# Kernel tuning notes

Measured on AMD Instinct MI355X. Metric: run time of the kernel, lower is better.

## Reference

```python
import jax, jax.numpy as jnp
import numpy as np

N = 50000   # graph nodes (== num_edges of road network, Embedding vocab)
E = 800000  # message-passing edges
F = 64      # static_feat_dim
H = 256     # hidden_dim
ID = 32     # id_embed_dim
DYN = 16    # dyn_feat_dim
B = 256
T = 128
STEPS = 3   # gcn_iter


def setup_inputs():
    key = jax.random.key(0)
    it = iter(jax.random.split(key, 48))

    def nrm(shape, fan_in):
        return jax.random.normal(next(it), shape, jnp.float32) / np.sqrt(fan_in)

    edge_src = jax.random.randint(next(it), (E,), 0, N)
    edge_dst = jax.random.randint(next(it), (E,), 0, N)
    lengths = jax.random.randint(next(it), (B,), T // 2, T + 1)
    traj = jax.random.randint(next(it), (B, T), 1, N)
    mask = jnp.arange(T)[None, :] < lengths[:, None]
    traj = jnp.where(mask, traj, 0)  # padding idx 0 past length
    x0 = jax.random.normal(next(it), (N, F), jnp.float32)
    dyn_feat = jax.random.normal(next(it), (B, DYN), jnp.float32)
    Din = H + ID + DYN
    z = lambda *s: jnp.zeros(s, jnp.float32)
    inp = dict(
        x0=x0, dyn_feat=dyn_feat,
        Wproj=nrm((F, H), F), bproj=z(H),
        Wz=nrm((F + H, H), F + H), bz=z(H),
        Wr=nrm((F + H, H), F + H), br=z(H),
        Wn=nrm((F + H, H), F + H), bn=z(H),
        id_emb=nrm((N, ID), 1.0).at[0].set(0.0),  # padding_idx=0
        film_W1=nrm((DYN, H), DYN), film_b1=z(H),
        film_W2=nrm((H, 2 * H), H), film_b2=z(2 * H),
        gru_Wi_f=nrm((Din, 3 * H), Din), gru_Wh_f=nrm((H, 3 * H), H),
        gru_bi_f=z(3 * H), gru_bh_f=z(3 * H),
        gru_Wi_b=nrm((Din, 3 * H), Din), gru_Wh_b=nrm((H, 3 * H), H),
        gru_bi_b=z(3 * H), gru_bh_b=z(3 * H),
        ln_g=jnp.ones((2 * H,), jnp.float32), ln_b=z(2 * H),
        attn_W1=nrm((2 * H + DYN, H), 2 * H + DYN), attn_b1=z(H),
        attn_W2=nrm((H, 1), H), attn_b2=z(1),
        gate_W=nrm((4 * H + DYN, 2 * H), 4 * H + DYN), gate_b=z(2 * H),
        fc_W1=nrm((2 * H + DYN, H), 2 * H + DYN), fc_b1=z(H),
        fc_W2=nrm((H, 1), H), fc_b2=z(1),
        traj=traj, lengths=lengths, edge_src=edge_src, edge_dst=edge_dst)
    return inp


def _run_gru(x, mask, Wi, Wh, bi, bh):
    # x: [B,T,D]; mask: [B,T] bool. Returns (outs [B,T,H] zeroed past length,
    # h_last [B,H] = state at last valid step), matching packed torch GRU.
    xg = jnp.einsum('btd,dh->bth', x, Wi) + bi  # precompute input gates
    Hd = Wh.shape[0]

    def step(h, inp):
        gx, m = inp
        gh = h @ Wh + bh
        xr, xz, xn = jnp.split(gx, 3, axis=-1)
        hr, hz, hn = jnp.split(gh, 3, axis=-1)
        r = jax.nn.sigmoid(xr + hr)
        zt = jax.nn.sigmoid(xz + hz)
        n = jnp.tanh(xn + r * hn)
        h_new = (1 - zt) * n + zt * h
        m2 = m[:, None]
        h = jnp.where(m2, h_new, h)
        return h, h * m2

    h0 = jnp.zeros((x.shape[0], Hd), x.dtype)
    h_last, outs = jax.lax.scan(step, h0, (jnp.swapaxes(xg, 0, 1), mask.T))
    return jnp.swapaxes(outs, 0, 1), h_last


def _forward(x0, dyn_feat, Wproj, bproj, Wz, bz, Wr, br, Wn, bn, id_emb,
             film_W1, film_b1, film_W2, film_b2,
             gru_Wi_f, gru_Wh_f, gru_bi_f, gru_bh_f,
             gru_Wi_b, gru_Wh_b, gru_bi_b, gru_bh_b,
             ln_g, ln_b, attn_W1, attn_b1, attn_W2, attn_b2,
             gate_W, gate_b, fc_W1, fc_b1, fc_W2, fc_b2,
             traj, lengths, edge_src, edge_dst):
    # --- GGNN message passing: scatter-add aggregation + gated update ---
    h = jnp.tanh(x0 @ Wproj + bproj)  # [N,H]
    for _ in range(STEPS):
        h_agg = jax.ops.segment_sum(h[edge_src], edge_dst, num_segments=N)
        xc = jnp.concatenate([x0, h_agg], axis=1)
        zg = jax.nn.sigmoid(xc @ Wz + bz)
        rg = jax.nn.sigmoid(xc @ Wr + br)
        h_t = jnp.tanh(jnp.concatenate([x0, rg * h_agg], axis=1) @ Wn + bn)
        h = (1 - zg) * h_agg + zg * h_t
    # --- FiLM-modulated trajectory sequence ---
    x_seq = h[traj]  # [B,T,H]
    film = jnp.tanh((dyn_feat @ film_W1 + film_b1) @ film_W2 + film_b2)
    g, b = jnp.split(film, 2, axis=-1)
    x_seq = x_seq * (1 + g[:, None, :]) + b[:, None, :]
    dyn_exp = jnp.broadcast_to(dyn_feat[:, None, :], (B, T, DYN))
    rnn_in = jnp.concatenate([x_seq, id_emb[traj], dyn_exp], axis=-1)
    mask = jnp.arange(T)[None, :] < lengths[:, None]
    # --- BiGRU over packed (length-masked) sequences ---
    out_f, h_f = _run_gru(rnn_in, mask, gru_Wi_f, gru_Wh_f, gru_bi_f, gru_bh_f)
    rev = jnp.maximum(lengths[:, None] - 1 - jnp.arange(T)[None, :], 0)  # [B,T]
    x_rev = jnp.take_along_axis(rnn_in, rev[..., None], axis=1)
    out_rb, h_b = _run_gru(x_rev, mask, gru_Wi_b, gru_Wh_b, gru_bi_b, gru_bh_b)
    out_b = jnp.take_along_axis(out_rb, rev[..., None], axis=1) * mask[..., None]
    rnn_out = jnp.concatenate([out_f, out_b], axis=-1)  # [B,T,2H]
    h_last = jnp.concatenate([h_f, h_b], axis=1)        # [B,2H]
    mu = h_last.mean(-1, keepdims=True)
    var = ((h_last - mu) ** 2).mean(-1, keepdims=True)
    rnn_last = (h_last - mu) / jnp.sqrt(var + 1e-5) * ln_g + ln_b
    # --- attention pooling over valid steps ---
    score_in = jnp.concatenate([rnn_out, dyn_exp], axis=-1)
    scores = (jnp.tanh(score_in @ attn_W1 + attn_b1) @ attn_W2 + attn_b2)[..., 0]
    scores = jnp.where(traj != 0, scores, -1e9)
    alpha = jax.nn.softmax(scores, axis=1)[..., None]
    context = (rnn_out * alpha).sum(axis=1)
    # --- fusion gate + head ---
    gate_in = jnp.concatenate([context, rnn_last, dyn_feat], axis=1)
    zf = jax.nn.sigmoid(gate_in @ gate_W + gate_b)
    final = zf * context + (1 - zf) * rnn_last
    hfc = jax.nn.gelu(jnp.concatenate([final, dyn_feat], axis=1) @ fc_W1 + fc_b1,
                      approximate=False)
    return (hfc @ fc_W2 + fc_b2)[:, 0]


def reference(x0, dyn_feat, Wproj, bproj, Wz, bz, Wr, br, Wn, bn, id_emb,
              film_W1, film_b1, film_W2, film_b2,
              gru_Wi_f, gru_Wh_f, gru_bi_f, gru_bh_f,
              gru_Wi_b, gru_Wh_b, gru_bi_b, gru_bh_b,
              ln_g, ln_b, attn_W1, attn_b1, attn_W2, attn_b2,
              gate_W, gate_b, fc_W1, fc_b1, fc_W2, fc_b2,
              traj, lengths, edge_src, edge_dst):
    return _forward(x0, dyn_feat, Wproj, bproj, Wz, bz, Wr, br, Wn, bn, id_emb,
                    film_W1, film_b1, film_W2, film_b2,
                    gru_Wi_f, gru_Wh_f, gru_bi_f, gru_bh_f,
                    gru_Wi_b, gru_Wh_b, gru_bi_b, gru_bh_b,
                    ln_g, ln_b, attn_W1, attn_b1, attn_W2, attn_b2,
                    gate_W, gate_b, fc_W1, fc_b1, fc_W2, fc_b2,
                    traj, lengths, edge_src, edge_dst)
```

## Files before the change

kernel.cpp:

```cpp
#include <hip/hip_runtime.h>
#include <hip/hip_fp16.h>
#include <cmath>

#define NN   50000
#define EE   800000
#define FF   64
#define HH   256
#define IDD  32
#define DYNN 16
#define BB   256
#define TT   128
#define DIN  304
#define G3   768
#define NQ   (HH/4)
#define NQG  ((FF+HH)/4)
#define NQX  (DIN/4)

typedef _Float16 h2_t __attribute__((ext_vector_type(2)));
__device__ __forceinline__ float sigf(float x){ return 1.0f/(1.0f+expf(-x)); }
__device__ __forceinline__ float fdot2(__half2 a, __half2 b, float c) {
    return __builtin_amdgcn_fdot2(*reinterpret_cast<h2_t*>(&a),
                                  *reinterpret_cast<h2_t*>(&b), c, false);
}

#define NPB 16
__global__ __launch_bounds__(256) void k_proj(
    const float* __restrict__ x0, const float* __restrict__ Wproj,
    const float* __restrict__ bproj, float* __restrict__ h,
    __half* __restrict__ h16)
{
    __shared__ float xs[NPB][FF];
    int n0 = blockIdx.x * NPB;
    int j  = threadIdx.x;
    for (int i = j; i < NPB*FF; i += 256) {
        int m = i / FF, k = i % FF;
        int n = n0 + m;
        xs[m][k] = (n < NN) ? x0[n*FF + k] : 0.f;
    }
    __syncthreads();
    float acc[NPB];
#pragma unroll
    for (int m = 0; m < NPB; ++m) acc[m] = 0.f;
    for (int k = 0; k < FF; ++k) {
        float w = Wproj[k*HH + j];
#pragma unroll
        for (int m = 0; m < NPB; ++m) acc[m] += xs[m][k]*w;
    }
    float b = bproj[j];
#pragma unroll
    for (int m = 0; m < NPB; ++m) {
        int n = n0 + m;
        if (n < NN) {
            float v = tanhf(acc[m] + b);
            h[(size_t)n*HH + j] = v;
            h16[(size_t)n*HH + j] = __float2half(v);
        }
    }
}

__global__ __launch_bounds__(768) void k_wt2(
    const float* __restrict__ Wh, __half2* __restrict__ Wq)
{
    int q = blockIdx.x;
    int j = threadIdx.x;
    float w0 = Wh[(size_t)(4*q+0)*G3 + j];
    float w1 = Wh[(size_t)(4*q+1)*G3 + j];
    float w2 = Wh[(size_t)(4*q+2)*G3 + j];
    float w3 = Wh[(size_t)(4*q+3)*G3 + j];
    Wq[((size_t)q*G3 + j)*2 + 0] = __floats2half2_rn(w0, w1);
    Wq[((size_t)q*G3 + j)*2 + 1] = __floats2half2_rn(w2, w3);
}

__global__ __launch_bounds__(256) void k_wtg(
    const float* __restrict__ W, float2* __restrict__ Wq)
{
    int q = blockIdx.x;
    int j = threadIdx.x;
    __half2 a = __floats2half2_rn(W[(size_t)(4*q+0)*HH + j], W[(size_t)(4*q+1)*HH + j]);
    __half2 b = __floats2half2_rn(W[(size_t)(4*q+2)*HH + j], W[(size_t)(4*q+3)*HH + j]);
    float2 o;
    reinterpret_cast<__half2*>(&o)[0] = a;
    reinterpret_cast<__half2*>(&o)[1] = b;
    Wq[(size_t)q*HH + j] = o;
}

__global__ __launch_bounds__(768) void k_wti(
    const float* __restrict__ Wi, float2* __restrict__ Wq)
{
    int q = blockIdx.x;
    int j = threadIdx.x;
    __half2 a = __floats2half2_rn(Wi[(size_t)(4*q+0)*G3 + j], Wi[(size_t)(4*q+1)*G3 + j]);
    __half2 b = __floats2half2_rn(Wi[(size_t)(4*q+2)*G3 + j], Wi[(size_t)(4*q+3)*G3 + j]);
    float2 o;
    reinterpret_cast<__half2*>(&o)[0] = a;
    reinterpret_cast<__half2*>(&o)[1] = b;
    Wq[(size_t)q*G3 + j] = o;
}

__global__ __launch_bounds__(256) void k_hist(
    const int* __restrict__ dst, int* __restrict__ cnt)
{
    int e = blockIdx.x*256 + threadIdx.x;
    if (e < EE) atomicAdd(&cnt[dst[e]], 1);
}

__global__ __launch_bounds__(1024) void k_prefix(
    const int* __restrict__ cnt, int* __restrict__ offs)
{
    __shared__ int sm[1024];
    __shared__ int carry;
    int j = threadIdx.x;
    if (j == 0) carry = 0;
    __syncthreads();
    for (int base = 0; base < NN; base += 1024) {
        int v = (base + j < NN) ? cnt[base + j] : 0;
        sm[j] = v; __syncthreads();
        for (int s = 1; s < 1024; s <<= 1) {
            int t = (j >= s) ? sm[j - s] : 0;
            __syncthreads();
            sm[j] += t;
            __syncthreads();
        }
        int inc = sm[j];
        int c = carry;
        if (base + j < NN) offs[base + j] = c + inc - v;
        __syncthreads();
        if (j == 1023) carry = c + sm[1023];
        __syncthreads();
    }
    if (j == 0) offs[NN] = carry;
}

__global__ __launch_bounds__(256) void k_fill(
    const int* __restrict__ src, const int* __restrict__ dst,
    const int* __restrict__ offs, int* __restrict__ cur,
    int* __restrict__ srcb)
{
    int e = blockIdx.x*256 + threadIdx.x;
    if (e < EE) {
        int d = dst[e];
        int p = atomicAdd(&cur[d], 1);
        srcb[offs[d] + p] = src[e];
    }
}

#define APB 4
__global__ __launch_bounds__(256) void k_aggregate(
    const __half* __restrict__ h16, const int* __restrict__ offs,
    const int* __restrict__ srcb, float* __restrict__ hagg)
{
    int w    = threadIdx.x >> 6;
    int lane = threadIdx.x & 63;
    int half = lane >> 5;
    int l32  = lane & 31;
    int n = blockIdx.x * APB + w;
    if (n >= NN) return;
    int e0 = offs[n], e1 = offs[n+1];
    float acc[8];
#pragma unroll
    for (int k = 0; k < 8; ++k) acc[k] = 0.f;
    int e = e0;
    for (; e + 8 <= e1; e += 8) {
        int sA = srcb[e     + half];
        int sB = srcb[e + 2 + half];
        int sC = srcb[e + 4 + half];
        int sD = srcb[e + 6 + half];
        float4 rA = *reinterpret_cast<const float4*>(&h16[(size_t)sA*HH + l32*8]);
        float4 rB = *reinterpret_cast<const float4*>(&h16[(size_t)sB*HH + l32*8]);
        float4 rC = *reinterpret_cast<const float4*>(&h16[(size_t)sC*HH + l32*8]);
        float4 rD = *reinterpret_cast<const float4*>(&h16[(size_t)sD*HH + l32*8]);
        const __half2* hA = reinterpret_cast<const __half2*>(&rA);
        const __half2* hB = reinterpret_cast<const __half2*>(&rB);
        const __half2* hC = reinterpret_cast<const __half2*>(&rC);
        const __half2* hD = reinterpret_cast<const __half2*>(&rD);
#pragma unroll
        for (int k = 0; k < 4; ++k) {
            float2 a = __half22float2(hA[k]);
            float2 b = __half22float2(hB[k]);
            float2 c = __half22float2(hC[k]);
            float2 d = __half22float2(hD[k]);
            acc[2*k]   += (a.x + b.x) + (c.x + d.x);
            acc[2*k+1] += (a.y + b.y) + (c.y + d.y);
        }
    }
    for (; e + 2 <= e1; e += 2) {
        int s = srcb[e + half];
        float4 r = *reinterpret_cast<const float4*>(&h16[(size_t)s*HH + l32*8]);
        const __half2* hp = reinterpret_cast<const __half2*>(&r);
#pragma unroll
        for (int k = 0; k < 4; ++k) {
            float2 a = __half22float2(hp[k]);
            acc[2*k] += a.x; acc[2*k+1] += a.y;
        }
    }
    if (e < e1 && half == 0) {
        int s = srcb[e];
        float4 r = *reinterpret_cast<const float4*>(&h16[(size_t)s*HH + l32*8]);
        const __half2* hp = reinterpret_cast<const __half2*>(&r);
#pragma unroll
        for (int k = 0; k < 4; ++k) {
            float2 a = __half22float2(hp[k]);
            acc[2*k] += a.x; acc[2*k+1] += a.y;
        }
    }
#pragma unroll
    for (int k = 0; k < 8; ++k) acc[k] += __shfl_xor(acc[k], 32, 64);
    if (half == 0) {
        float4 o0 = {acc[0], acc[1], acc[2], acc[3]};
        float4 o1 = {acc[4], acc[5], acc[6], acc[7]};
        float4* dst = reinterpret_cast<float4*>(&hagg[(size_t)n*HH + l32*8]);
        dst[0] = o0; dst[1] = o1;
    }
}

__global__ __launch_bounds__(256) void k_gnn_update(
    const float* __restrict__ x0, const float* __restrict__ hagg,
    const float2* __restrict__ wqz, const float2* __restrict__ wqr,
    const float2* __restrict__ wqn,
    const float* __restrict__ bz, const float* __restrict__ br,
    const float* __restrict__ bn, float* __restrict__ h,
    __half* __restrict__ h16)
{
    __shared__ __align__(16) __half inh[NPB][FF+HH];
    __shared__ __align__(16) __half rhh[NPB][HH];
    __shared__ float hsf[NPB][HH];
    int n0 = blockIdx.x * NPB;
    int j  = threadIdx.x;
    for (int i = j; i < NPB*FF; i += 256) {
        int m = i >> 6, k = i & 63;
        int n = n0 + m;
        inh[m][k] = __float2half((n < NN) ? x0[n*FF + k] : 0.f);
    }
#pragma unroll
    for (int m = 0; m < NPB; ++m) {
        int n = n0 + m;
        float hv = (n < NN) ? hagg[(size_t)n*HH + j] : 0.f;
        hsf[m][j] = hv;
        inh[m][FF + j] = __float2half(hv);
    }
    __syncthreads();

    float az[NPB], ar[NPB];
#pragma unroll
    for (int m = 0; m < NPB; ++m) { az[m] = 0.f; ar[m] = 0.f; }
    for (int q = 0; q < NQG; ++q) {
        float2 wzr = wqz[(size_t)q*HH + j];
        float2 wrr = wqr[(size_t)q*HH + j];
        __half2 wz01 = reinterpret_cast<__half2*>(&wzr)[0];
        __half2 wz23 = reinterpret_cast<__half2*>(&wzr)[1];
        __half2 wr01 = reinterpret_cast<__half2*>(&wrr)[0];
        __half2 wr23 = reinterpret_cast<__half2*>(&wrr)[1];
#pragma unroll
        for (int m = 0; m < NPB; ++m) {
            float2 hraw = *reinterpret_cast<const float2*>(&inh[m][4*q]);
            __half2 h01 = reinterpret_cast<__half2*>(&hraw)[0];
            __half2 h23 = reinterpret_cast<__half2*>(&hraw)[1];
            az[m] = fdot2(h01, wz01, az[m]); az[m] = fdot2(h23, wz23, az[m]);
            ar[m] = fdot2(h01, wr01, ar[m]); ar[m] = fdot2(h23, wr23, ar[m]);
        }
    }
    float bzj = bz[j], brj = br[j];
    float zg[NPB];
#pragma unroll
    for (int m = 0; m < NPB; ++m) {
        zg[m] = sigf(az[m] + bzj);
        float rg = sigf(ar[m] + brj);
        rhh[m][j] = __float2half(rg * hsf[m][j]);
    }
    __syncthreads();
    float an[NPB];
#pragma unroll
    for (int m = 0; m < NPB; ++m) an[m] = 0.f;
    for (int q = 0; q < FF/4; ++q) {
        float2 wnr = wqn[(size_t)q*HH + j];
        __half2 wn01 = reinterpret_cast<__half2*>(&wnr)[0];
        __half2 wn23 = reinterpret_cast<__half2*>(&wnr)[1];
#pragma unroll
        for (int m = 0; m < NPB; ++m) {
            float2 hraw = *reinterpret_cast<const float2*>(&inh[m][4*q]);
            __half2 h01 = reinterpret_cast<__half2*>(&hraw)[0];
            __half2 h23 = reinterpret_cast<__half2*>(&hraw)[1];
            an[m] = fdot2(h01, wn01, an[m]); an[m] = fdot2(h23, wn23, an[m]);
        }
    }
    for (int q = FF/4; q < NQG; ++q) {
        float2 wnr = wqn[(size_t)q*HH + j];
        __half2 wn01 = reinterpret_cast<__half2*>(&wnr)[0];
        __half2 wn23 = reinterpret_cast<__half2*>(&wnr)[1];
#pragma unroll
        for (int m = 0; m < NPB; ++m) {
            float2 hraw = *reinterpret_cast<const float2*>(&rhh[m][4*q - FF]);
            __half2 h01 = reinterpret_cast<__half2*>(&hraw)[0];
            __half2 h23 = reinterpret_cast<__half2*>(&hraw)[1];
            an[m] = fdot2(h01, wn01, an[m]); an[m] = fdot2(h23, wn23, an[m]);
        }
    }
    float bnj = bn[j];
#pragma unroll
    for (int m = 0; m < NPB; ++m) {
        int n = n0 + m;
        if (n < NN) {
            float ht = tanhf(an[m] + bnj);
            float hv = (1.f - zg[m])*hsf[m][j] + zg[m]*ht;
            h[(size_t)n*HH + j] = hv;
            h16[(size_t)n*HH + j] = __float2half(hv);
        }
    }
}

__global__ __launch_bounds__(256) void k_film(
    const float* __restrict__ dyn, const float* __restrict__ W1,
    const float* __restrict__ b1, const float* __restrict__ W2,
    const float* __restrict__ b2, float* __restrict__ film)
{
    __shared__ float t1[HH];
    __shared__ float ds[DYNN];
    int b = blockIdx.x, j = threadIdx.x;
    if (j < DYNN) ds[j] = dyn[b*DYNN + j];
    __syncthreads();
    float acc = b1[j];
    for (int k = 0; k < DYNN; ++k) acc += ds[k]*W1[k*HH + j];
    t1[j] = acc;
    __syncthreads();
    float a0 = b2[j], a1 = b2[HH + j];
    for (int k = 0; k < HH; ++k) {
        float t = t1[k];
        a0 += t * W2[k*2*HH + j];
        a1 += t * W2[k*2*HH + HH + j];
    }
    film[b*2*HH + j]      = tanhf(a0);
    film[b*2*HH + HH + j] = tanhf(a1);
}

#define RPB 16
#define XGBLK ((BB*TT)/RPB)
__global__ __launch_bounds__(256) void k_xg2(
    const float* __restrict__ hfin, const float* __restrict__ id_emb,
    const float* __restrict__ dyn,  const float* __restrict__ film,
    const int* __restrict__ traj,   const int* __restrict__ lengths,
    const float2* __restrict__ Wqi_f, const float* __restrict__ bi_f,
    const float2* __restrict__ Wqi_b, const float* __restrict__ bi_b,
    __half* __restrict__ xg_f, __half* __restrict__ xg_b)
{
    __shared__ __align__(16) __half in[RPB][DIN];
    int dir = blockIdx.x / XGBLK;
    int r0  = (blockIdx.x - dir*XGBLK) * RPB;
    const float2* Wq = dir ? Wqi_b : Wqi_f;
    const float* bi = dir ? bi_b : bi_f;
    __half* xg = dir ? xg_b : xg_f;
    int j  = threadIdx.x;
#pragma unroll
    for (int m = 0; m < RPB; ++m) {
        int r = r0 + m;
        int b = r >> 7, t = r & 127;
        int tt = t;
        if (dir) { int L = lengths[b]; tt = L - 1 - t; if (tt < 0) tt = 0; }
        int idx = traj[b*TT + tt];
        float g  = film[b*2*HH + j];
        float bf = film[b*2*HH + HH + j];
        in[m][j] = __float2half(hfin[(size_t)idx*HH + j]*(1.f + g) + bf);
        if (j < IDD)               in[m][HH + j] = __float2half(id_emb[(size_t)idx*IDD + j]);
        else if (j < IDD + DYNN)   in[m][HH + IDD + (j - IDD)] = __float2half(dyn[b*DYNN + (j - IDD)]);
    }
    __syncthreads();
    float a0[RPB], a1[RPB], a2[RPB];
#pragma unroll
    for (int m = 0; m < RPB; ++m) { a0[m] = 0.f; a1[m] = 0.f; a2[m] = 0.f; }
    for (int q = 0; q < NQX; ++q) {
        float2 w0r = Wq[(size_t)q*G3 + j];
        float2 w1r = Wq[(size_t)q*G3 + HH + j];
        float2 w2r = Wq[(size_t)q*G3 + 2*HH + j];
        __half2 w0a = reinterpret_cast<__half2*>(&w0r)[0];
        __half2 w0b = reinterpret_cast<__half2*>(&w0r)[1];
        __half2 w1a = reinterpret_cast<__half2*>(&w1r)[0];
        __half2 w1b = reinterpret_cast<__half2*>(&w1r)[1];
        __half2 w2a = reinterpret_cast<__half2*>(&w2r)[0];
        __half2 w2b = reinterpret_cast<__half2*>(&w2r)[1];
#pragma unroll
        for (int m = 0; m < RPB; ++m) {
            float2 hraw = *reinterpret_cast<const float2*>(&in[m][4*q]);
            __half2 h01 = reinterpret_cast<__half2*>(&hraw)[0];
            __half2 h23 = reinterpret_cast<__half2*>(&hraw)[1];
            a0[m] = fdot2(h01, w0a, a0[m]); a0[m] = fdot2(h23, w0b, a0[m]);
            a1[m] = fdot2(h01, w1a, a1[m]); a1[m] = fdot2(h23, w1b, a1[m]);
            a2[m] = fdot2(h01, w2a, a2[m]); a2[m] = fdot2(h23, w2b, a2[m]);
        }
    }
    float bi0 = bi[j], bi1 = bi[HH + j], bi2 = bi[2*HH + j];
#pragma unroll
    for (int m = 0; m < RPB; ++m) {
        __half* o = &xg[(size_t)(r0 + m)*G3];
        o[j]        = __float2half(a0[m] + bi0);
        o[HH + j]   = __float2half(a1[m] + bi1);
        o[2*HH + j] = __float2half(a2[m] + bi2);
    }
}

#define NBS 2
#define SCBLK (BB/NBS)
#define LQ 24
__global__ __launch_bounds__(768, 3) void k_scan2(
    const __half* __restrict__ xg_f, const __half* __restrict__ xg_b,
    const __half2* __restrict__ Wq_f, const float* __restrict__ bh_f,
    const __half2* __restrict__ Wq_b, const float* __restrict__ bh_b,
    const int* __restrict__ lengths,
    float* __restrict__ out_f, float* __restrict__ out_b,
    float* __restrict__ h_last)
{
    __shared__ float hsh[NBS][HH];
    __shared__ __align__(16) __half hshh[NBS][HH];
    __shared__ float gh[NBS][G3];
    __shared__ __align__(16) float2 lw[LQ][G3];
    int dir  = blockIdx.x / SCBLK;
    int bblk = blockIdx.x - dir*SCBLK;
    const __half* xg = dir ? xg_b : xg_f;
    const __half2* Wq = dir ? Wq_b : Wq_f;
    const float* bh = dir ? bh_b : bh_f;
    float* out = dir ? out_b : out_f;
    int b0 = bblk * NBS;
    int j  = threadIdx.x;
    int m  = j >> 8;
    int jj = j & 255;
    if (j < NBS*HH) { hsh[j >> 8][j & 255] = 0.f; hshh[j >> 8][j & 255] = __float2half(0.f); }
    int L0 = lengths[b0], L1 = lengths[b0 + 1];
    float bhj = bh[j];
    const float2* wqp = reinterpret_cast<const float2*>(Wq) + j;
#pragma unroll
    for (int q = 0; q < LQ; ++q) lw[q][j] = wqp[(size_t)q*G3];
    __syncthreads();
    for (int t = 0; t < TT; ++t) {
        float xrv = 0.f, xzv = 0.f, xnv = 0.f;
        if (j < NBS*HH) {
            const __half* xr = &xg[((size_t)(b0 + m)*TT + t)*G3];
            xrv = __half2float(xr[jj]);
            xzv = __half2float(xr[HH + jj]);
            xnv = __half2float(xr[2*HH + jj]);
        }
        float a0 = bhj, a1 = bhj;
#pragma unroll
        for (int p = 0; p < LQ/2; ++p) {
            float4 h0raw = *reinterpret_cast<const float4*>(&hshh[0][8*p]);
            float4 h1raw = *reinterpret_cast<const float4*>(&hshh[1][8*p]);
            const __half2* h0 = reinterpret_cast<const __half2*>(&h0raw);
            const __half2* h1 = reinterpret_cast<const __half2*>(&h1raw);
            float2 w0 = lw[2*p][j], w1 = lw[2*p+1][j];
            const __half2* wA = reinterpret_cast<const __half2*>(&w0);
            const __half2* wB = reinterpret_cast<const __half2*>(&w1);
            a0 = fdot2(h0[0], wA[0], a0); a0 = fdot2(h0[1], wA[1], a0);
            a0 = fdot2(h0[2], wB[0], a0); a0 = fdot2(h0[3], wB[1], a0);
            a1 = fdot2(h1[0], wA[0], a1); a1 = fdot2(h1[1], wA[1], a1);
            a1 = fdot2(h1[2], wB[0], a1); a1 = fdot2(h1[3], wB[1], a1);
        }
#pragma unroll
        for (int p = LQ/2; p < NQ/2; ++p) {
            float4 h0raw = *reinterpret_cast<const float4*>(&hshh[0][8*p]);
            float4 h1raw = *reinterpret_cast<const float4*>(&hshh[1][8*p]);
            const __half2* h0 = reinterpret_cast<const __half2*>(&h0raw);
            const __half2* h1 = reinterpret_cast<const __half2*>(&h1raw);
            float2 w0 = wqp[(size_t)(2*p)*G3], w1 = wqp[(size_t)(2*p+1)*G3];
            const __half2* wA = reinterpret_cast<const __half2*>(&w0);
            const __half2* wB = reinterpret_cast<const __half2*>(&w1);
            a0 = fdot2(h0[0], wA[0], a0); a0 = fdot2(h0[1], wA[1], a0);
            a0 = fdot2(h0[2], wB[0], a0); a0 = fdot2(h0[3], wB[1], a0);
            a1 = fdot2(h1[0], wA[0], a1); a1 = fdot2(h1[1], wA[1], a1);
            a1 = fdot2(h1[2], wB[0], a1); a1 = fdot2(h1[3], wB[1], a1);
        }
        gh[0][j] = a0; gh[1][j] = a1;
        __syncthreads();
        if (j < NBS*HH) {
            int b = b0 + m;
            int L = m ? L1 : L0;
            float gr = sigf(xrv + gh[m][jj]);
            float gz = sigf(xzv + gh[m][HH + jj]);
            float gn = tanhf(xnv + gr*gh[m][2*HH + jj]);
            float hold = hsh[m][jj];
            float hnew = (1.f - gz)*gn + gz*hold;
            if (t < L) {
                hsh[m][jj] = hnew;
                hshh[m][jj] = __float2half(hnew);
                if (!dir) out[((size_t)b*TT + t)*HH + jj] = hnew;
                else      out[((size_t)b*TT + (L-1-t))*HH + jj] = hnew;
            } else if (!dir) {
                out[((size_t)b*TT + t)*HH + jj] = 0.f;
            }
        }
        __syncthreads();
    }
    if (j < NBS*HH) {
        int b = b0 + m;
        int L = m ? L1 : L0;
        h_last[b*2*HH + (dir ? HH : 0) + jj] = hsh[m][jj];
        if (dir) {
            for (int t = L; t < TT; ++t) out[((size_t)b*TT + t)*HH + jj] = 0.f;
        }
    }
}

#define SPB 16
#define SCD 528
__global__ __launch_bounds__(256) void k_scores(
    const float* __restrict__ out_f, const float* __restrict__ out_b,
    const float* __restrict__ dyn,   const int* __restrict__ traj,
    const float* __restrict__ W1,    const float* __restrict__ b1,
    const float* __restrict__ W2,    const float* __restrict__ b2,
    float* __restrict__ scores)
{
    __shared__ float in[SPB][SCD];
    __shared__ float part[4][SPB];
    int r0 = blockIdx.x * SPB;
    int j  = threadIdx.x;
    int lane = j & 63, wid = j >> 6;
#pragma unroll
    for (int m = 0; m < SPB; ++m) {
        int r = r0 + m;
        int b = r >> 7;
        in[m][j]      = out_f[(size_t)r*HH + j];
        in[m][HH + j] = out_b[(size_t)r*HH + j];
        if (j < DYNN) in[m][2*HH + j] = dyn[b*DYNN + j];
    }
    __syncthreads();
    float acc[SPB];
#pragma unroll
    for (int m = 0; m < SPB; ++m) acc[m] = 0.f;
    for (int k = 0; k < SCD; ++k) {
        float w = W1[k*HH + j];
#pragma unroll
        for (int m = 0; m < SPB; ++m) acc[m] += in[m][k]*w;
    }
    float b1j = b1[j], w2j = W2[j];
#pragma unroll
    for (int m = 0; m < SPB; ++m) {
        float s = tanhf(acc[m] + b1j) * w2j;
#pragma unroll
        for (int off = 32; off > 0; off >>= 1) s += __shfl_xor(s, off, 64);
        if (lane == 0) part[wid][m] = s;
    }
    __syncthreads();
    if (j < SPB) {
        int r = r0 + j;
        int b = r >> 7, t = r & 127;
        float s = part[0][j] + part[1][j] + part[2][j] + part[3][j];
        scores[r] = (traj[b*TT + t] != 0) ? (s + b2[0]) : -1e9f;
    }
}

__global__ __launch_bounds__(256) void k_context(
    const float* __restrict__ scores, const float* __restrict__ out_f,
    const float* __restrict__ out_b,  float* __restrict__ context)
{
    __shared__ float al[TT];
    __shared__ float red[256];
    int b = blockIdx.x, j = threadIdx.x;
    float s = (j < TT) ? scores[b*TT + j] : -INFINITY;
    red[j] = s; __syncthreads();
    for (int t = 128; t > 0; t >>= 1) { if (j < t) red[j] = fmaxf(red[j], red[j+t]); __syncthreads(); }
    float mx = red[0]; __syncthreads();
    float e = (j < TT) ? expf(s - mx) : 0.f;
    red[j] = e; __syncthreads();
    for (int t = 128; t > 0; t >>= 1) { if (j < t) red[j] += red[j+t]; __syncthreads(); }
    float tot = red[0];
    if (j < TT) al[j] = e / tot;
    __syncthreads();
    float c0 = 0.f, c1 = 0.f;
    for (int t = 0; t < TT; ++t) {
        float a = al[t];
        c0 += a * out_f[((size_t)b*TT + t)*HH + j];
        c1 += a * out_b[((size_t)b*TT + t)*HH + j];
    }
    context[b*2*HH + j]      = c0;
    context[b*2*HH + HH + j] = c1;
}

__global__ __launch_bounds__(256) void k_head(
    const float* __restrict__ h_last, const float* __restrict__ context,
    const float* __restrict__ dyn,    const float* __restrict__ ln_g,
    const float* __restrict__ ln_b,   const float* __restrict__ gate_W,
    const float* __restrict__ gate_b, const float* __restrict__ fc_W1,
    const float* __restrict__ fc_b1,  const float* __restrict__ fc_W2,
    const float* __restrict__ fc_b2,  float* __restrict__ outp)
{
    __shared__ float gi[1040];
    __shared__ float fin[SCD];
    __shared__ float red[256];
    int b = blockIdx.x, j = threadIdx.x;
    float h0 = h_last[b*2*HH + j], h1 = h_last[b*2*HH + HH + j];
    red[j] = h0 + h1; __syncthreads();
    for (int s = 128; s > 0; s >>= 1) { if (j < s) red[j] += red[j+s]; __syncthreads(); }
    float mu = red[0] / 512.f; __syncthreads();
    float d0 = h0 - mu, d1 = h1 - mu;
    red[j] = d0*d0 + d1*d1; __syncthreads();
    for (int s = 128; s > 0; s >>= 1) { if (j < s) red[j] += red[j+s]; __syncthreads(); }
    float inv = rsqrtf(red[0] / 512.f + 1e-5f); __syncthreads();
    gi[2*HH + j]      = d0*inv*ln_g[j]      + ln_b[j];
    gi[2*HH + HH + j] = d1*inv*ln_g[HH + j] + ln_b[HH + j];
    gi[j]      = context[b*2*HH + j];
    gi[HH + j] = context[b*2*HH + HH + j];
    if (j < DYNN) gi[1024 + j] = dyn[b*DYNN + j];
    __syncthreads();
    float a0 = gate_b[j], a1 = gate_b[HH + j];
    for (int k = 0; k < 1040; ++k) {
        float x = gi[k];
        a0 += x * gate_W[k*2*HH + j];
        a1 += x * gate_W[k*2*HH + HH + j];
    }
    float z0 = sigf(a0), z1 = sigf(a1);
    fin[j]      = z0*gi[j]      + (1.f - z0)*gi[2*HH + j];
    fin[HH + j] = z1*gi[HH + j] + (1.f - z1)*gi[2*HH + HH + j];
    if (j < DYNN) fin[2*HH + j] = gi[1024 + j];
    __syncthreads();
    float acc = fc_b1[j];
    for (int k = 0; k < SCD; ++k) acc += fin[k]*fc_W1[k*HH + j];
    float x = acc;
    float hfc = 0.5f * x * (1.f + erff(x * 0.70710678118654752f));
    red[j] = hfc * fc_W2[j]; __syncthreads();
    for (int s = 128; s > 0; s >>= 1) { if (j < s) red[j] += red[j+s]; __syncthreads(); }
    if (j == 0) outp[b] = red[0] + fc_b2[0];
}

extern "C" void kernel_launch(void* const* d_in, const int* in_sizes, int n_in,
                              void* d_out, int out_size, void* d_ws, size_t ws_size,
                              hipStream_t stream)
{
    const float* x0      = (const float*)d_in[0];
    const float* dyn     = (const float*)d_in[1];
    const float* Wproj   = (const float*)d_in[2];
    const float* bproj   = (const float*)d_in[3];
    const float* Wz      = (const float*)d_in[4];
    const float* bz      = (const float*)d_in[5];
    const float* Wr      = (const float*)d_in[6];
    const float* br      = (const float*)d_in[7];
    const float* Wn      = (const float*)d_in[8];
    const float* bn      = (const float*)d_in[9];
    const float* id_emb  = (const float*)d_in[10];
    const float* film_W1 = (const float*)d_in[11];
    const float* film_b1 = (const float*)d_in[12];
    const float* film_W2 = (const float*)d_in[13];
    const float* film_b2 = (const float*)d_in[14];
    const float* gWi_f   = (const float*)d_in[15];
    const float* gWh_f   = (const float*)d_in[16];
    const float* gbi_f   = (const float*)d_in[17];
    const float* gbh_f   = (const float*)d_in[18];
    const float* gWi_b   = (const float*)d_in[19];
    const float* gWh_b   = (const float*)d_in[20];
    const float* gbi_b   = (const float*)d_in[21];
    const float* gbh_b   = (const float*)d_in[22];
    const float* ln_g    = (const float*)d_in[23];
    const float* ln_b    = (const float*)d_in[24];
    const float* attn_W1 = (const float*)d_in[25];
    const float* attn_b1 = (const float*)d_in[26];
    const float* attn_W2 = (const float*)d_in[27];
    const float* attn_b2 = (const float*)d_in[28];
    const float* gate_W  = (const float*)d_in[29];
    const float* gate_b  = (const float*)d_in[30];
    const float* fc_W1   = (const float*)d_in[31];
    const float* fc_b1   = (const float*)d_in[32];
    const float* fc_W2   = (const float*)d_in[33];
    const float* fc_b2   = (const float*)d_in[34];
    const int*   traj    = (const int*)d_in[35];
    const int*   lengths = (const int*)d_in[36];
    const int*   e_src   = (const int*)d_in[37];
    const int*   e_dst   = (const int*)d_in[38];

    float* ws = (float*)d_ws;
    const size_t off_h      = 0;
    const size_t off_hagg   = (size_t)NN*HH;
    const size_t off_xgf    = off_hagg;
    const size_t off_xgb    = off_xgf + (size_t)BB*TT*G3/2;
    const size_t off_outf   = 0;
    const size_t off_outb   = off_xgb + (size_t)BB*TT*G3/2;
    const size_t off_film   = off_outb + (size_t)BB*TT*HH;
    const size_t off_hlast  = off_film + (size_t)BB*2*HH;
    const size_t off_scores = off_hlast + (size_t)BB*2*HH;
    const size_t off_ctx    = off_scores + (size_t)BB*TT;
    const size_t off_wqf    = off_ctx + (size_t)BB*2*HH;
    const size_t off_wqb    = off_wqf + (size_t)NQ*G3*2;
    const size_t off_wqz    = off_wqb + (size_t)NQ*G3*2;
    const size_t off_wqr    = off_wqz + (size_t)NQG*HH*2;
    const size_t off_wqn    = off_wqr + (size_t)NQG*HH*2;
    const size_t off_wif    = off_wqn + (size_t)NQG*HH*2;
    const size_t off_wib    = off_wif + (size_t)NQX*G3*2;
    const size_t off_h16    = 27000000;

    float*   h      = ws + off_h;
    float*   hagg   = ws + off_hagg;
    __half*  xg_f   = (__half*)(ws + off_xgf);
    __half*  xg_b   = (__half*)(ws + off_xgb);
    float*   out_f  = ws + off_outf;
    float*   out_b  = ws + off_outb;
    float*   film   = ws + off_film;
    float*   hlast  = ws + off_hlast;
    float*   scores = ws + off_scores;
    float*   ctx    = ws + off_ctx;
    __half2* wq_f   = (__half2*)(ws + off_wqf);
    __half2* wq_b   = (__half2*)(ws + off_wqb);
    float2*  wqz    = (float2*)(ws + off_wqz);
    float2*  wqr    = (float2*)(ws + off_wqr);
    float2*  wqn    = (float2*)(ws + off_wqn);
    float2*  wqi_f  = (float2*)(ws + off_wif);
    float2*  wqi_b  = (float2*)(ws + off_wib);
    __half*  h16    = (__half*)(ws + off_h16);

    int* cnt  = (int*)(ws + off_hagg + (size_t)NN*HH);
    int* cur  = cnt + NN;
    int* offs = cur + NN;
    int* srcb = offs + NN + 1;

    k_proj<<<(NN + NPB - 1)/NPB, 256, 0, stream>>>(x0, Wproj, bproj, h, h16);

    k_wt2<<<NQ, 768, 0, stream>>>(gWh_f, wq_f);
    k_wt2<<<NQ, 768, 0, stream>>>(gWh_b, wq_b);
    k_wtg<<<NQG, 256, 0, stream>>>(Wz, wqz);
    k_wtg<<<NQG, 256, 0, stream>>>(Wr, wqr);
    k_wtg<<<NQG, 256, 0, stream>>>(Wn, wqn);
    k_wti<<<NQX, 768, 0, stream>>>(gWi_f, wqi_f);
    k_wti<<<NQX, 768, 0, stream>>>(gWi_b, wqi_b);

    hipMemsetAsync(cnt, 0, 2*(size_t)NN*sizeof(int), stream);
    k_hist<<<(EE + 255)/256, 256, 0, stream>>>(e_dst, cnt);
    k_prefix<<<1, 1024, 0, stream>>>(cnt, offs);
    k_fill<<<(EE + 255)/256, 256, 0, stream>>>(e_src, e_dst, offs, cur, srcb);

    for (int step = 0; step < 3; ++step) {
        k_aggregate<<<(NN + APB - 1)/APB, 256, 0, stream>>>(h16, offs, srcb, hagg);
        k_gnn_update<<<(NN + NPB - 1)/NPB, 256, 0, stream>>>(
            x0, hagg, wqz, wqr, wqn, bz, br, bn, h, h16);
    }

    k_film<<<BB, 256, 0, stream>>>(dyn, film_W1, film_b1, film_W2, film_b2, film);

    k_xg2<<<2*XGBLK, 256, 0, stream>>>(h, id_emb, dyn, film, traj, lengths,
                                       wqi_f, gbi_f, wqi_b, gbi_b, xg_f, xg_b);

    k_scan2<<<2*SCBLK, 768, 0, stream>>>(xg_f, xg_b, wq_f, gbh_f, wq_b, gbh_b,
                                         lengths, out_f, out_b, hlast);

    k_scores<<<(BB*TT)/SPB, 256, 0, stream>>>(out_f, out_b, dyn, traj,
                                              attn_W1, attn_b1, attn_W2, attn_b2, scores);
    k_context<<<BB, 256, 0, stream>>>(scores, out_f, out_b, ctx);
    k_head<<<BB, 256, 0, stream>>>(hlast, ctx, dyn, ln_g, ln_b, gate_W, gate_b,
                                   fc_W1, fc_b1, fc_W2, fc_b2, (float*)d_out);
}
```

Before: 2.306 ms.

## Process four sequences per GRU scan block and drop shared-memory weight cache

Each scan block now handles four batch rows instead of two, so every recurrent weight load from global memory is reused across four hidden states. The partial LDS caching of the recurrent weights is removed, and all weights are streamed from global/L2 every timestep. This halves the number of scan blocks and doubles per-thread accumulator work, trading parallelism for weight reuse. The gate update loop is reorganised so 512 threads each cover two sequences.

```diff
diff --git a/kernel.cpp b/kernel.cpp
--- a/kernel.cpp
+++ b/kernel.cpp
@@ -396,9 +396,8 @@
     }
 }
 
-#define NBS 2
+#define NBS 4
 #define SCBLK (BB/NBS)
-#define LQ 24
 __global__ __launch_bounds__(768, 3) void k_scan2(
     const __half* __restrict__ xg_f, const __half* __restrict__ xg_b,
     const __half2* __restrict__ Wq_f, const float* __restrict__ bh_f,
@@ -410,7 +409,6 @@
     __shared__ float hsh[NBS][HH];
     __shared__ __align__(16) __half hshh[NBS][HH];
     __shared__ float gh[NBS][G3];
-    __shared__ __align__(16) float2 lw[LQ][G3];
     int dir  = blockIdx.x / SCBLK;
     int bblk = blockIdx.x - dir*SCBLK;
     const __half* xg = dir ? xg_b : xg_f;
@@ -419,44 +417,42 @@
     float* out = dir ? out_b : out_f;
     int b0 = bblk * NBS;
     int j  = threadIdx.x;
-    int m  = j >> 8;
     int jj = j & 255;
-    if (j < NBS*HH) { hsh[j >> 8][j & 255] = 0.f; hshh[j >> 8][j & 255] = __float2half(0.f); }
-    int L0 = lengths[b0], L1 = lengths[b0 + 1];
+    int m0 = j >> 8;
+    for (int i = j; i < NBS*HH; i += 768) {
+        hsh[i >> 8][i & 255] = 0.f;
+        hshh[i >> 8][i & 255] = __float2half(0.f);
+    }
+    int Ls[NBS];
+#pragma unroll
+    for (int s = 0; s < NBS; ++s) Ls[s] = lengths[b0 + s];
     float bhj = bh[j];
     const float2* wqp = reinterpret_cast<const float2*>(Wq) + j;
-#pragma unroll
-    for (int q = 0; q < LQ; ++q) lw[q][j] = wqp[(size_t)q*G3];
     __syncthreads();
     for (int t = 0; t < TT; ++t) {
-        float xrv = 0.f, xzv = 0.f, xnv = 0.f;
-        if (j < NBS*HH) {
-            const __half* xr = &xg[((size_t)(b0 + m)*TT + t)*G3];
-            xrv = __half2float(xr[jj]);
-            xzv = __half2float(xr[HH + jj]);
-            xnv = __half2float(xr[2*HH + jj]);
-        }
-        float a0 = bhj, a1 = bhj;
-#pragma unroll
-        for (int p = 0; p < LQ/2; ++p) {
+        float xr0 = 0.f, xz0 = 0.f, xn0 = 0.f;
+        float xr1 = 0.f, xz1 = 0.f, xn1 = 0.f;
+        if (j < 512) {
+            const __half* xa = &xg[((size_t)(b0 + m0)*TT + t)*G3];
+            const __half* xb = &xg[((size_t)(b0 + m0 + 2)*TT + t)*G3];
+            xr0 = __half2float(xa[jj]);
+            xz0 = __half2float(xa[HH + jj]);
+            xn0 = __half2float(xa[2*HH + jj]);
+            xr1 = __half2float(xb[jj]);
+            xz1 = __half2float(xb[HH + jj]);
+            xn1 = __half2float(xb[2*HH + jj]);
+        }
+        float a0 = bhj, a1 = bhj, a2 = bhj, a3 = bhj;
+#pragma unroll
+        for (int p = 0; p < NQ/2; ++p) {
             float4 h0raw = *reinterpret_cast<const float4*>(&hshh[0][8*p]);
             float4 h1raw = *reinterpret_cast<const float4*>(&hshh[1][8*p]);
+            float4 h2raw = *reinterpret_cast<const float4*>(&hshh[2][8*p]);
+            float4 h3raw = *reinterpret_cast<const float4*>(&hshh[3][8*p]);
             const __half2* h0 = reinterpret_cast<const __half2*>(&h0raw);
             const __half2* h1 = reinterpret_cast<const __half2*>(&h1raw);
-            float2 w0 = lw[2*p][j], w1 = lw[2*p+1][j];
-            const __half2* wA = reinterpret_cast<const __half2*>(&w0);
-            const __half2* wB = reinterpret_cast<const __half2*>(&w1);
-            a0 = fdot2(h0[0], wA[0], a0); a0 = fdot2(h0[1], wA[1], a0);
-            a0 = fdot2(h0[2], wB[0], a0); a0 = fdot2(h0[3], wB[1], a0);
-            a1 = fdot2(h1[0], wA[0], a1); a1 = fdot2(h1[1], wA[1], a1);
-            a1 = fdot2(h1[2], wB[0], a1); a1 = fdot2(h1[3], wB[1], a1);
-        }
-#pragma unroll
-        for (int p = LQ/2; p < NQ/2; ++p) {
-            float4 h0raw = *reinterpret_cast<const float4*>(&hshh[0][8*p]);
-            float4 h1raw = *reinterpret_cast<const float4*>(&hshh[1][8*p]);
-            const __half2* h0 = reinterpret_cast<const __half2*>(&h0raw);
-            const __half2* h1 = reinterpret_cast<const __half2*>(&h1raw);
+            const __half2* h2 = reinterpret_cast<const __half2*>(&h2raw);
+            const __half2* h3 = reinterpret_cast<const __half2*>(&h3raw);
             float2 w0 = wqp[(size_t)(2*p)*G3], w1 = wqp[(size_t)(2*p+1)*G3];
             const __half2* wA = reinterpret_cast<const __half2*>(&w0);
             const __half2* wB = reinterpret_cast<const __half2*>(&w1);
@@ -464,34 +460,49 @@
             a0 = fdot2(h0[2], wB[0], a0); a0 = fdot2(h0[3], wB[1], a0);
             a1 = fdot2(h1[0], wA[0], a1); a1 = fdot2(h1[1], wA[1], a1);
             a1 = fdot2(h1[2], wB[0], a1); a1 = fdot2(h1[3], wB[1], a1);
-        }
-        gh[0][j] = a0; gh[1][j] = a1;
+            a2 = fdot2(h2[0], wA[0], a2); a2 = fdot2(h2[1], wA[1], a2);
+            a2 = fdot2(h2[2], wB[0], a2); a2 = fdot2(h2[3], wB[1], a2);
+            a3 = fdot2(h3[0], wA[0], a3); a3 = fdot2(h3[1], wA[1], a3);
+            a3 = fdot2(h3[2], wB[0], a3); a3 = fdot2(h3[3], wB[1], a3);
+        }
+        gh[0][j] = a0; gh[1][j] = a1; gh[2][j] = a2; gh[3][j] = a3;
         __syncthreads();
-        if (j < NBS*HH) {
-            int b = b0 + m;
-            int L = m ? L1 : L0;
-            float gr = sigf(xrv + gh[m][jj]);
-            float gz = sigf(xzv + gh[m][HH + jj]);
-            float gn = tanhf(xnv + gr*gh[m][2*HH + jj]);
-            float hold = hsh[m][jj];
-            float hnew = (1.f - gz)*gn + gz*hold;
-            if (t < L) {
-                hsh[m][jj] = hnew;
-                hshh[m][jj] = __float2half(hnew);
-                if (!dir) out[((size_t)b*TT + t)*HH + jj] = hnew;
-                else      out[((size_t)b*TT + (L-1-t))*HH + jj] = hnew;
-            } else if (!dir) {
-                out[((size_t)b*TT + t)*HH + jj] = 0.f;
+        if (j < 512) {
+#pragma unroll
+            for (int ss = 0; ss < 2; ++ss) {
+                int s = m0 + 2*ss;
+                int b = b0 + s;
+                int L = Ls[s];
+                float xr = ss ? xr1 : xr0;
+                float xz = ss ? xz1 : xz0;
+                float xn = ss ? xn1 : xn0;
+                float gr = sigf(xr + gh[s][jj]);
+                float gz = sigf(xz + gh[s][HH + jj]);
+                float gn = tanhf(xn + gr*gh[s][2*HH + jj]);
+                float hold = hsh[s][jj];
+                float hnew = (1.f - gz)*gn + gz*hold;
+                if (t < L) {
+                    hsh[s][jj] = hnew;
+                    hshh[s][jj] = __float2half(hnew);
+                    if (!dir) out[((size_t)b*TT + t)*HH + jj] = hnew;
+                    else      out[((size_t)b*TT + (L-1-t))*HH + jj] = hnew;
+                } else if (!dir) {
+                    out[((size_t)b*TT + t)*HH + jj] = 0.f;
+                }
             }
         }
         __syncthreads();
     }
-    if (j < NBS*HH) {
-        int b = b0 + m;
-        int L = m ? L1 : L0;
-        h_last[b*2*HH + (dir ? HH : 0) + jj] = hsh[m][jj];
-        if (dir) {
-            for (int t = L; t < TT; ++t) out[((size_t)b*TT + t)*HH + jj] = 0.f;
+    if (j < 512) {
+#pragma unroll
+        for (int ss = 0; ss < 2; ++ss) {
+            int s = m0 + 2*ss;
+            int b = b0 + s;
+            int L = Ls[s];
+            h_last[b*2*HH + (dir ? HH : 0) + jj] = hsh[s][jj];
+            if (dir) {
+                for (int t = L; t < TT; ++t) out[((size_t)b*TT + t)*HH + jj] = 0.f;
+            }
         }
     }
 }
```

New measurement: 2.699 ms. 1.17x slower.
